# Kernel optimization log

Measured on AMD Instinct MI355X. Metric: run time of the kernel, lower is better.

Reference implementation:

```python
import jax, jax.numpy as jnp
import numpy as np

EPS = 1e-06


def setup_inputs() -> dict:
    key = jax.random.key(0)
    k1, k2, k3 = jax.random.split(key, 3)
    N, L, H, D = 2, 2048, 8, 64
    return {
        "queries": jax.random.normal(k1, (N, L, H, D), dtype=jnp.float32),
        "keys": jax.random.normal(k2, (N, L, H, D), dtype=jnp.float32),
        "values": jax.random.normal(k3, (N, L, H, D), dtype=jnp.float32),
    }


def reference(queries, keys, values):
    # [N, L, H, D] -> [N, H, L, D]
    q = jnp.transpose(queries, (0, 2, 1, 3))
    k = jnp.transpose(keys, (0, 2, 1, 3))
    v = jnp.transpose(values, (0, 2, 1, 3))
    # kernel_method = sigmoid (applied to q and k only)
    q = jax.nn.sigmoid(q)
    k = jax.nn.sigmoid(k)
    L = q.shape[2]
    normal = (jnp.arange(L, dtype=q.dtype) + 1.0)[None, None, :]  # [1,1,L]

    sink_incoming = 1.0 / jnp.einsum('nhld,nhld->nhl', q + EPS, jnp.cumsum(k, axis=2) + EPS)
    source_outgoing = 1.0 / jnp.einsum('nhld,nhld->nhl', k + EPS, jnp.cumsum(q, axis=2) + EPS)
    sink_incoming = sink_incoming * normal
    source_outgoing = source_outgoing * normal

    conserved_sink = jnp.einsum(
        'nhld,nhld->nhl', q + EPS,
        jnp.cumsum(k * source_outgoing[..., None], axis=2) + EPS) / normal
    conserved_source = jnp.einsum(
        'nhld,nhld->nhl', k + EPS,
        jnp.cumsum(q * sink_incoming[..., None], axis=2) + EPS) / normal
    conserved_source = jnp.clip(conserved_source, -1.0, 1.0)

    sink_allocation = jax.nn.sigmoid(conserved_sink)
    conserved_source = jnp.exp(conserved_source)
    source_competition = conserved_source / jnp.cumsum(conserved_source, axis=-1) * normal

    # causal dot product: outer-product cumsum as in the original
    q_scaled = q * (sink_incoming / normal)[..., None]
    v_scaled = v * source_competition[..., None]
    kv = jnp.cumsum(jnp.einsum('nhld,nhlm->nhldm', k, v_scaled), axis=2)  # [N,H,L,D,M]
    qkv = jnp.einsum('nhld,nhldm->nhlm', q_scaled, kv)
    x = qkv * sink_allocation[..., None]
    # back to [N, L, H, M]
    return jnp.transpose(x, (0, 2, 1, 3))
```

## Files before the change

### kernel.cpp

```cpp
#include <hip/hip_runtime.h>
#include <math.h>

constexpr int Nn = 2, Hh = 8, Ll = 2048, Dd = 64;
constexpr int S  = Nn * Hh;
constexpr int C  = 64;
constexpr int NC = Ll / C;
constexpr int SC = S * NC;

constexpr int SB  = 72;
constexpr int SRP = 65;
constexpr int SS8 = 9;

#define EPSF 1e-6f
#define FLAG_MAGIC 0x5F3A9D21u

typedef __attribute__((ext_vector_type(8))) short short8;
typedef __attribute__((ext_vector_type(4))) float f32x4;
#define MFMA16(a, b, c) __builtin_amdgcn_mfma_f32_16x16x32_bf16(a, b, c, 0, 0, 0)

__device__ __forceinline__ float rcpf(float x) { return __builtin_amdgcn_rcpf(x); }
__device__ __forceinline__ float sigf(float x) { return rcpf(1.0f + __expf(-x)); }

__device__ __forceinline__ float waveRed(float v) {
#pragma unroll
    for (int off = 32; off > 0; off >>= 1) v += __shfl_xor(v, off, 64);
    return v;
}

__device__ __forceinline__ int gidx(int n, int l, int h, int d) {
    return ((n * Ll + l) * Hh + h) * Dd + d;
}

__device__ __forceinline__ float fc(const float4& v, int u) { return ((const float*)&v)[u]; }

__device__ __forceinline__ unsigned short f2bf(float x) {
    unsigned int u = __float_as_uint(x);
    unsigned int r = (u + 0x7fffu + ((u >> 16) & 1u)) >> 16;
    return (unsigned short)r;
}
__device__ __forceinline__ unsigned int pack2(float lo, float hi) {
    return (unsigned int)f2bf(lo) | ((unsigned int)f2bf(hi) << 16);
}
__device__ __forceinline__ float bf2f(unsigned short u) {
    return __uint_as_float(((unsigned int)u) << 16);
}
__device__ __forceinline__ float lo16(unsigned int x) { return __uint_as_float(x << 16); }
__device__ __forceinline__ float hi16(unsigned int x) { return __uint_as_float(x & 0xffff0000u); }
__device__ __forceinline__ void unpack8(const uint4& v, float* o) {
    o[0] = lo16(v.x); o[1] = hi16(v.x); o[2] = lo16(v.y); o[3] = hi16(v.y);
    o[4] = lo16(v.z); o[5] = hi16(v.z); o[6] = lo16(v.w); o[7] = hi16(v.w);
}

__device__ __forceinline__ void pubf(float* p, float v) {
    __hip_atomic_store((unsigned int*)p, __float_as_uint(v),
                       __ATOMIC_RELAXED, __HIP_MEMORY_SCOPE_AGENT);
}
__device__ __forceinline__ float rdf(const float* p) {
    return __uint_as_float(__hip_atomic_load((const unsigned int*)p,
                       __ATOMIC_RELAXED, __HIP_MEMORY_SCOPE_AGENT));
}
__device__ __forceinline__ void pubu(unsigned int* p, unsigned int v) {
    __hip_atomic_store(p, v, __ATOMIC_RELAXED, __HIP_MEMORY_SCOPE_AGENT);
}
__device__ __forceinline__ unsigned long long rd64(const void* p) {
    return __hip_atomic_load((const unsigned long long*)p,
                             __ATOMIC_RELAXED, __HIP_MEMORY_SCOPE_AGENT);
}
__device__ __forceinline__ void publish_flag(unsigned int* f, int t) {
    asm volatile("s_waitcnt vmcnt(0)" ::: "memory");
    __syncthreads();
    if (t == 0)
        __hip_atomic_store(f, FLAG_MAGIC, __ATOMIC_RELAXED, __HIP_MEMORY_SCOPE_AGENT);
}
__device__ __forceinline__ void wait_n(const unsigned int* f, int n, int t) {
    if (t < 64) {
        const bool need = (t < n);
        for (;;) {
            unsigned int v = need
                ? __hip_atomic_load(&f[t], __ATOMIC_RELAXED, __HIP_MEMORY_SCOPE_AGENT)
                : FLAG_MAGIC;
            if (__all(v == FLAG_MAGIC)) break;
            __builtin_amdgcn_s_sleep(8);
        }
    }
    __syncthreads();
    asm volatile("" ::: "memory");
}

__global__ __launch_bounds__(256, 2) void k_all(
        const float* __restrict__ Q, const float* __restrict__ K,
        const float* __restrict__ V,
        float* __restrict__ SK, float* __restrict__ SQ,
        float* __restrict__ SKso, float* __restrict__ SQsi,
        float* __restrict__ KVT, unsigned short* __restrict__ KVpb,
        float* __restrict__ Out,
        unsigned int* __restrict__ f0, unsigned int* __restrict__ f1,
        unsigned long long* __restrict__ f2, unsigned int* __restrict__ f3,
        unsigned int* __restrict__ f4) {
    __shared__ __align__(16) unsigned short sqB[C * SB];
    __shared__ __align__(16) unsigned short skB[C * SB];
    __shared__ __align__(16) unsigned short vsT[C * SB];
    __shared__ __align__(16) unsigned short stB[C * SB];
    __shared__ __align__(16) float Pun[4608];
    __shared__ float scrA[C * SS8], scrB[C * SS8];
    __shared__ float colK[C], colQ[C], pk[Dd], pq[Dd];
    __shared__ float lsi[C], lso[C], rw1[C], rw2[C], le[C], ecum[C], lsc[C], s2l[C];
    __shared__ float pcsv;

    const int b = blockIdx.x, s = b / NC, c = b % NC;
    const int n = s / Hh, h = s % Hh, t = threadIdx.x;
    const int w = t >> 6, lane = t & 63, mf = lane & 15, qq = lane >> 4;
    const int I0 = 16 * w;
    float* P = Pun;

    {
        int d0 = (4 * t) & 63, ig = t >> 4;
        float psk[4] = {0, 0, 0, 0}, psq[4] = {0, 0, 0, 0};
#pragma unroll
        for (int j = 0; j < 4; j++) {
            int i = ig + 16 * j;
            int id = gidx(n, c * C + i, h, d0);
            float4 q4 = *(const float4*)&Q[id];
            float4 k4 = *(const float4*)&K[id];
            float a0 = sigf(q4.x), a1 = sigf(q4.y), a2 = sigf(q4.z), a3 = sigf(q4.w);
            float b0 = sigf(k4.x), b1 = sigf(k4.y), b2 = sigf(k4.z), b3 = sigf(k4.w);
            *(uint2*)&sqB[i * SB + d0] = make_uint2(pack2(a0, a1), pack2(a2, a3));
            *(uint2*)&skB[i * SB + d0] = make_uint2(pack2(b0, b1), pack2(b2, b3));
            psq[0] += a0; psq[1] += a1; psq[2] += a2; psq[3] += a3;
            psk[0] += b0; psk[1] += b1; psk[2] += b2; psk[3] += b3;
        }
#pragma unroll
        for (int r = 0; r < 4; r++) {
            P[ig * 64 + d0 + r] = psk[r];
            P[1024 + ig * 64 + d0 + r] = psq[r];
        }
        int i0 = (t & 15) * 4, dt = (t >> 4) * 4;
        float4 vr[4];
#pragma unroll
        for (int r = 0; r < 4; r++)
            vr[r] = *(const float4*)&V[gidx(n, c * C + i0 + r, h, dt)];
#pragma unroll
        for (int u = 0; u < 4; u++)
            *(uint2*)&vsT[(dt + u) * SB + i0] = make_uint2(
                pack2(fc(vr[0], u), fc(vr[1], u)), pack2(fc(vr[2], u), fc(vr[3], u)));
    }
    __syncthreads();
    if (t < 64) {
        float v = 0.f;
#pragma unroll
        for (int g = 0; g < 16; g++) v += P[g * 64 + t];
        pubf(&SK[b * 64 + t], v);
    } else if (t < 128) {
        int d = t - 64; float v = 0.f;
#pragma unroll
        for (int g = 0; g < 16; g++) v += P[1024 + g * 64 + d];
        pubf(&SQ[b * 64 + d], v);
    }
    publish_flag(&f0[b], t);

    wait_n(&f0[s * NC], c, t);

    {
        int d = t & 63, g = t >> 6;
        float pa = 0.f, pb = 0.f;
#pragma unroll
        for (int u = 0; u < 8; u++) {
            int cp = g + 4 * u;
            float va = rdf(&SK[(s * NC + cp) * 64 + d]);
            float vb = rdf(&SQ[(s * NC + cp) * 64 + d]);
            pa += (cp < c) ? va : 0.f;
            pb += (cp < c) ? vb : 0.f;
        }
        P[2048 + g * 64 + d] = pa;
        P[2304 + g * 64 + d] = pb;
    }
#pragma unroll
    for (int j = 0; j < 2; j++) {
        int flat = 8 * t + 2048 * j, i = flat >> 6, d0 = flat & 63;
        uint4 xq = *(const uint4*)&sqB[i * SB + d0];
        uint4 xk = *(const uint4*)&skB[i * SB + d0];
        float qa[8], ka[8];
        unpack8(xq, qa); unpack8(xk, ka);
        float sq = 0.f, sk = 0.f;
#pragma unroll
        for (int u = 0; u < 8; u++) { sq += qa[u]; sk += ka[u]; }
        scrB[i * SS8 + (d0 >> 3)] = sq;
        scrA[i * SS8 + (d0 >> 3)] = sk;
    }
    __syncthreads();
    if (t < 64) {
        float v = 0.f;
#pragma unroll
        for (int u = 0; u < 8; u++) v += scrA[t * SS8 + u];
        colK[t] = v;
    } else if (t < 128) {
        int i = t - 64; float v = 0.f;
#pragma unroll
        for (int u = 0; u < 8; u++) v += scrB[i * SS8 + u];
        colQ[i] = v;
    } else if (t < 192) {
        int d = t - 128;
        pk[d] = P[2048 + d] + P[2112 + d] + P[2176 + d] + P[2240 + d];
    } else {
        int d = t - 192;
        pq[d] = P[2304 + d] + P[2368 + d] + P[2432 + d] + P[2496 + d];
    }
    __syncthreads();

    {
        f32x4 acc[4] = {{0,0,0,0},{0,0,0,0},{0,0,0,0},{0,0,0,0}};
#pragma unroll
        for (int kk = 0; kk < 64; kk += 32) {
            short8 a = *(const short8*)&sqB[(I0 + mf) * SB + kk + qq * 8];
#pragma unroll
            for (int J = 0; J < 4; J++) {
                short8 bb = *(const short8*)&skB[(16 * J + mf) * SB + kk + qq * 8];
                acc[J] = MFMA16(a, bb, acc[J]);
            }
        }
#pragma unroll
        for (int J = 0; J < 4; J++)
#pragma unroll
            for (int r = 0; r < 4; r++)
                P[(I0 + 4 * qq + r) * SRP + 16 * J + mf] = acc[J][r];
    }
    __syncthreads();

    {
        int i = t >> 2, g = t & 3, l = c * C + i;
        float prow[16], pcol[16];
        float r1 = 0.f, r2 = 0.f;
#pragma unroll
        for (int u = 0; u < 16; u++) {
            int jj = g + 4 * u;
            prow[u] = P[i * SRP + jj] + EPSF * colK[jj];
            pcol[u] = P[jj * SRP + i] + EPSF * colQ[jj];
            bool ok = (jj <= i);
            r1 += ok ? prow[u] : 0.f;
            r2 += ok ? pcol[u] : 0.f;
        }
        float b1 = 0.f, b2 = 0.f;
#pragma unroll
        for (int u = 0; u < 16; u++) {
            int d = g * 16 + u;
            b1 += (bf2f(sqB[i * SB + d]) + EPSF) * (pk[d] + EPSF);
            b2 += (bf2f(skB[i * SB + d]) + EPSF) * (pq[d] + EPSF);
        }
        r1 += __shfl_xor(r1, 1, 64); r1 += __shfl_xor(r1, 2, 64);
        r2 += __shfl_xor(r2, 1, 64); r2 += __shfl_xor(r2, 2, 64);
        b1 += __shfl_xor(b1, 1, 64); b1 += __shfl_xor(b1, 2, 64);
        b2 += __shfl_xor(b2, 1, 64); b2 += __shfl_xor(b2, 2, 64);
        if (g == 0) {
            float nf = (float)(l + 1);
            lsi[i] = nf * rcpf(b1 + r1);
            lso[i] = nf * rcpf(b2 + r2);
        }
        __syncthreads();

        float a1 = 0.f, a2 = 0.f;
#pragma unroll
        for (int u = 0; u < 16; u++) {
            int jj = g + 4 * u;
            float t1 = lso[jj] * prow[u];
            float t2 = lsi[jj] * pcol[u];
            bool ok = (jj <= i);
            a1 += ok ? t1 : 0.f;
            a2 += ok ? t2 : 0.f;
        }
        a1 += __shfl_xor(a1, 1, 64); a1 += __shfl_xor(a1, 2, 64);
        a2 += __shfl_xor(a2, 1, 64); a2 += __shfl_xor(a2, 2, 64);
        if (g == 0) { rw1[i] = a1; rw2[i] = a2; }
    }
    {
        int d = t >> 2, g = t & 3;
        float v1 = 0.f, v2 = 0.f;
#pragma unroll
        for (int u = 0; u < 16; u++) {
            int i = g * 16 + u;
            v1 += bf2f(skB[i * SB + d]) * lso[i];
            v2 += bf2f(sqB[i * SB + d]) * lsi[i];
        }
        v1 += __shfl_xor(v1, 1, 64); v1 += __shfl_xor(v1, 2, 64);
        v2 += __shfl_xor(v2, 1, 64); v2 += __shfl_xor(v2, 2, 64);
        if (g == 0) {
            pubf(&SKso[b * 64 + d], v1);
            pubf(&SQsi[b * 64 + d], v2);
        }
    }
    publish_flag(&f1[b], t);

    wait_n(&f1[s * NC], c, t);

    {
        int d = t & 63, g = t >> 6;
        float pa = 0.f, pb = 0.f;
#pragma unroll
        for (int u = 0; u < 8; u++) {
            int cp = g + 4 * u;
            float va = rdf(&SKso[(s * NC + cp) * 64 + d]);
            float vb = rdf(&SQsi[(s * NC + cp) * 64 + d]);
            pa += (cp < c) ? va : 0.f;
            pb += (cp < c) ? vb : 0.f;
        }
        scrA[g * 64 + d] = pa;
        scrA[256 + g * 64 + d] = pb;
    }
    __syncthreads();
    if (t < 64) pk[t] = scrA[t] + scrA[64 + t] + scrA[128 + t] + scrA[192 + t];
    else if (t < 128) {
        int d = t - 64;
        pq[d] = scrA[256 + d] + scrA[320 + d] + scrA[384 + d] + scrA[448 + d];
    }
    __syncthreads();
    {
        int i = t >> 2, g = t & 3, l = c * C + i;
        float b1 = 0.f, b2 = 0.f;
#pragma unroll
        for (int j = 0; j < 2; j++) {
            uint4 xq = *(const uint4*)&sqB[i * SB + g * 16 + 8 * j];
            uint4 xk = *(const uint4*)&skB[i * SB + g * 16 + 8 * j];
            float qa[8], ka[8];
            unpack8(xq, qa); unpack8(xk, ka);
            int d = g * 16 + 8 * j;
#pragma unroll
            for (int u = 0; u < 8; u++) {
                b1 += (qa[u] + EPSF) * (pk[d + u] + EPSF);
                b2 += (ka[u] + EPSF) * (pq[d + u] + EPSF);
            }
        }
        b1 += __shfl_xor(b1, 1, 64); b1 += __shfl_xor(b1, 2, 64);
        b2 += __shfl_xor(b2, 1, 64); b2 += __shfl_xor(b2, 2, 64);
        if (g == 0) {
            float nf = (float)(l + 1);
            float cs  = (b1 + rw1[i]) * rcpf(nf);
            float csr = (b2 + rw2[i]) * rcpf(nf);
            csr = fminf(fmaxf(csr, -1.f), 1.f);
            float e = __expf(csr);
            float sal = sigf(cs);
            s2l[i] = lsi[i] * rcpf(nf) * sal;
            le[i] = e;
        }
    }
    __syncthreads();
    if (t < 64) {
        float run = le[t];
#pragma unroll
        for (int off = 1; off < 64; off <<= 1) {
            float o = __shfl_up(run, off, 64);
            if (t >= off) run += o;
        }
        ecum[t] = run;
    }
    __syncthreads();
    if (t == 0) {
        unsigned long long pv = ((unsigned long long)FLAG_MAGIC << 32)
                              | (unsigned long long)__float_as_uint(ecum[63]);
        __hip_atomic_store(&f2[b], pv, __ATOMIC_RELAXED, __HIP_MEMORY_SCOPE_AGENT);
    }

    if (t < 64) {
        bool need = (t < c);
        float tv = 0.f;
        for (;;) {
            unsigned long long x = need
                ? __hip_atomic_load(&f2[s * NC + t], __ATOMIC_RELAXED, __HIP_MEMORY_SCOPE_AGENT)
                : ((unsigned long long)FLAG_MAGIC << 32);
            if (__all((unsigned int)(x >> 32) == FLAG_MAGIC)) {
                tv = need ? __uint_as_float((unsigned int)x) : 0.f;
                break;
            }
            __builtin_amdgcn_s_sleep(8);
        }
        float v = waveRed(tv);
        if (t == 0) pcsv = v;
    }
    __syncthreads();

    if (t < 64) {
        int l = c * C + t;
        lsc[t] = le[t] * rcpf(pcsv + ecum[t]) * (float)(l + 1);
    }
    __syncthreads();

    {
        int i = t >> 2, g = t & 3;
        unsigned int wds[8];
#pragma unroll
        for (int p = 0; p < 8; p++) {
            int j0 = g * 16 + 2 * p;
            float v0 = (j0     <= i) ? P[i * SRP + j0]     * lsc[j0]     : 0.f;
            float v1 = (j0 + 1 <= i) ? P[i * SRP + j0 + 1] * lsc[j0 + 1] : 0.f;
            wds[p] = pack2(v0, v1);
        }
        *(uint4*)&stB[i * SB + g * 16]     = make_uint4(wds[0], wds[1], wds[2], wds[3]);
        *(uint4*)&stB[i * SB + g * 16 + 8] = make_uint4(wds[4], wds[5], wds[6], wds[7]);
    }
    __syncthreads();

    unsigned short* skT = (unsigned short*)Pun;
    unsigned short* vsV = (unsigned short*)(Pun + 2304);
#pragma unroll
    for (int j = 0; j < 2; j++) {
        int flat = 8 * t + 2048 * j, dR = flat >> 6, i0 = flat & 63;
        uint4 vv = *(const uint4*)&vsT[dR * SB + i0];
        float x[8];
        unpack8(vv, x);
#pragma unroll
        for (int u = 0; u < 8; u++) x[u] *= lsc[i0 + u];
        uint4 o;
        o.x = pack2(x[0], x[1]); o.y = pack2(x[2], x[3]);
        o.z = pack2(x[4], x[5]); o.w = pack2(x[6], x[7]);
        *(uint4*)&vsV[dR * SB + i0] = o;
    }
    {
        int i0 = (t & 15) * 4, dt = (t >> 4) * 4;
        uint2 kr[4];
#pragma unroll
        for (int r = 0; r < 4; r++) kr[r] = *(const uint2*)&skB[(i0 + r) * SB + dt];
#pragma unroll
        for (int u = 0; u < 4; u++) {
            unsigned int e0 = (u < 2 ? kr[0].x : kr[0].y), e1 = (u < 2 ? kr[1].x : kr[1].y);
            unsigned int e2 = (u < 2 ? kr[2].x : kr[2].y), e3 = (u < 2 ? kr[3].x : kr[3].y);
            int sh = (u & 1) * 16;
            unsigned int lo = ((e0 >> sh) & 0xffffu) | (((e1 >> sh) & 0xffffu) << 16);
            unsigned int hi = ((e2 >> sh) & 0xffffu) | (((e3 >> sh) & 0xffffu) << 16);
            *(uint2*)&skT[(dt + u) * SB + i0] = make_uint2(lo, hi);
        }
    }
    __syncthreads();

    {
        f32x4 acc[4] = {{0,0,0,0},{0,0,0,0},{0,0,0,0},{0,0,0,0}};
#pragma unroll
        for (int kk = 0; kk < 64; kk += 32) {
            short8 a = *(const short8*)&vsV[(I0 + mf) * SB + kk + qq * 8];
#pragma unroll
            for (int J = 0; J < 4; J++) {
                short8 bb = *(const short8*)&skT[(16 * J + mf) * SB + kk + qq * 8];
                acc[J] = MFMA16(a, bb, acc[J]);
            }
        }
#pragma unroll
        for (int J = 0; J < 4; J++)
#pragma unroll
            for (int r = 0; r < 4; r++)
                pubf(&KVT[(size_t)b * 4096 + (I0 + 4 * qq + r) * 64 + 16 * J + mf],
                     acc[J][r]);
    }
    publish_flag(&f3[b], t);

    if (c < 8) {
        wait_n(&f3[s * NC], NC, t);
        int e0 = c * 512 + 2 * t;
        float2 x[NC];
#pragma unroll
        for (int cp = 0; cp < NC; cp++) {
            unsigned long long v = rd64(&KVT[(size_t)(s * NC + cp) * 4096 + e0]);
            x[cp].x = __uint_as_float((unsigned int)v);
            x[cp].y = __uint_as_float((unsigned int)(v >> 32));
        }
        float r0 = 0.f, r1 = 0.f;
#pragma unroll
        for (int cp = 0; cp < NC; cp++) {
            pubu((unsigned int*)&KVpb[(size_t)(s * NC + cp) * 4096 + e0], pack2(r0, r1));
            r0 += x[cp].x; r1 += x[cp].y;
        }
        publish_flag(&f4[s * 8 + c], t);
    }

    wait_n(&f4[8 * s], 8, t);
    unsigned long long kvp[4];
    size_t base = (size_t)b * 4096;
#pragma unroll
    for (int j = 0; j < 2; j++) {
        kvp[2 * j]     = rd64(&KVpb[base + 8 * t + 2048 * j]);
        kvp[2 * j + 1] = rd64(&KVpb[base + 8 * t + 2048 * j + 4]);
    }
#pragma unroll
    for (int j = 0; j < 2; j++) {
        int flat = 8 * t + 2048 * j, i = flat >> 6, d0 = flat & 63;
        *(uint2*)&skB[i * SB + d0] =
            make_uint2((unsigned int)kvp[2 * j], (unsigned int)(kvp[2 * j] >> 32));
        *(uint2*)&skB[i * SB + d0 + 4] =
            make_uint2((unsigned int)kvp[2 * j + 1], (unsigned int)(kvp[2 * j + 1] >> 32));
    }
    __syncthreads();

    {
        f32x4 acc[4] = {{0,0,0,0},{0,0,0,0},{0,0,0,0},{0,0,0,0}};
#pragma unroll
        for (int kk = 0; kk < 64; kk += 32) {
            short8 a1 = *(const short8*)&sqB[(I0 + mf) * SB + kk + qq * 8];
            short8 a2 = *(const short8*)&stB[(I0 + mf) * SB + kk + qq * 8];
#pragma unroll
            for (int J = 0; J < 4; J++) {
                short8 b1 = *(const short8*)&skB[(16 * J + mf) * SB + kk + qq * 8];
                acc[J] = MFMA16(a1, b1, acc[J]);
                short8 b2 = *(const short8*)&vsT[(16 * J + mf) * SB + kk + qq * 8];
                acc[J] = MFMA16(a2, b2, acc[J]);
            }
        }
#pragma unroll
        for (int J = 0; J < 4; J++)
#pragma unroll
            for (int r = 0; r < 4; r++) {
                int io = I0 + 4 * qq + r;
                Out[gidx(n, c * C + io, h, 16 * J + mf)] = acc[J][r] * s2l[io];
            }
    }
}

extern "C" void kernel_launch(void* const* d_in, const int* in_sizes, int n_in,
                              void* d_out, int out_size, void* d_ws, size_t ws_size,
                              hipStream_t stream) {
    const float* Q = (const float*)d_in[0];
    const float* K = (const float*)d_in[1];
    const float* V = (const float*)d_in[2];
    float* Out = (float*)d_out;

    float* ws   = (float*)d_ws;
    float* SK   = ws;
    float* SQ   = SK   + SC * 64;
    float* SKso = SQ   + SC * 64;
    float* SQsi = SKso + SC * 64;
    float* KVT  = SQsi + SC * 64;
    unsigned short* KVpb = (unsigned short*)(KVT + (size_t)SC * 4096);
    unsigned long long* f2 = (unsigned long long*)(KVpb + (size_t)SC * 4096);
    unsigned int* f0 = (unsigned int*)(f2 + SC);
    unsigned int* f1 = f0 + SC;
    unsigned int* f3 = f1 + SC;
    unsigned int* f4 = f3 + SC;

    k_all<<<SC, 256, 0, stream>>>(Q, K, V, SK, SQ, SKso, SQsi, KVT, KVpb, Out,
                                  f0, f1, f2, f3, f4);
}
```

Before: 99.54 us.

## Overlap cross-block flag waits with independent local work

```diff
diff --git a/kernel.cpp b/kernel.cpp
--- a/kernel.cpp
+++ b/kernel.cpp
@@ -134,15 +134,6 @@
             P[ig * 64 + d0 + r] = psk[r];
             P[1024 + ig * 64 + d0 + r] = psq[r];
         }
-        int i0 = (t & 15) * 4, dt = (t >> 4) * 4;
-        float4 vr[4];
-#pragma unroll
-        for (int r = 0; r < 4; r++)
-            vr[r] = *(const float4*)&V[gidx(n, c * C + i0 + r, h, dt)];
-#pragma unroll
-        for (int u = 0; u < 4; u++)
-            *(uint2*)&vsT[(dt + u) * SB + i0] = make_uint2(
-                pack2(fc(vr[0], u), fc(vr[1], u)), pack2(fc(vr[2], u), fc(vr[3], u)));
     }
     __syncthreads();
     if (t < 64) {
@@ -158,22 +149,18 @@
     }
     publish_flag(&f0[b], t);
 
-    wait_n(&f0[s * NC], c, t);
-
-    {
-        int d = t & 63, g = t >> 6;
-        float pa = 0.f, pb = 0.f;
-#pragma unroll
-        for (int u = 0; u < 8; u++) {
-            int cp = g + 4 * u;
-            float va = rdf(&SK[(s * NC + cp) * 64 + d]);
-            float vb = rdf(&SQ[(s * NC + cp) * 64 + d]);
-            pa += (cp < c) ? va : 0.f;
-            pb += (cp < c) ? vb : 0.f;
-        }
-        P[2048 + g * 64 + d] = pa;
-        P[2304 + g * 64 + d] = pb;
-    }
+    {
+        int i0 = (t & 15) * 4, dt = (t >> 4) * 4;
+        float4 vr[4];
+#pragma unroll
+        for (int r = 0; r < 4; r++)
+            vr[r] = *(const float4*)&V[gidx(n, c * C + i0 + r, h, dt)];
+#pragma unroll
+        for (int u = 0; u < 4; u++)
+            *(uint2*)&vsT[(dt + u) * SB + i0] = make_uint2(
+                pack2(fc(vr[0], u), fc(vr[1], u)), pack2(fc(vr[2], u), fc(vr[3], u)));
+    }
+
 #pragma unroll
     for (int j = 0; j < 2; j++) {
         int flat = 8 * t + 2048 * j, i = flat >> 6, d0 = flat & 63;
@@ -198,12 +185,6 @@
 #pragma unroll
         for (int u = 0; u < 8; u++) v += scrB[i * SS8 + u];
         colQ[i] = v;
-    } else if (t < 192) {
-        int d = t - 128;
-        pk[d] = P[2048 + d] + P[2112 + d] + P[2176 + d] + P[2240 + d];
-    } else {
-        int d = t - 192;
-        pq[d] = P[2304 + d] + P[2368 + d] + P[2432 + d] + P[2496 + d];
     }
     __syncthreads();
 
@@ -226,51 +207,61 @@
     }
     __syncthreads();
 
-    {
-        int i = t >> 2, g = t & 3, l = c * C + i;
-        float prow[16], pcol[16];
-        float r1 = 0.f, r2 = 0.f;
+    const int bi = t >> 2, bg = t & 3, bl = c * C + bi;
+    float prow[16], pcol[16];
+    float r1 = 0.f, r2 = 0.f;
+#pragma unroll
+    for (int u = 0; u < 16; u++) {
+        int jj = bg + 4 * u;
+        prow[u] = P[bi * SRP + jj] + EPSF * colK[jj];
+        pcol[u] = P[jj * SRP + bi] + EPSF * colQ[jj];
+        bool ok = (jj <= bi);
+        r1 += ok ? prow[u] : 0.f;
+        r2 += ok ? pcol[u] : 0.f;
+    }
+    r1 += __shfl_xor(r1, 1, 64); r1 += __shfl_xor(r1, 2, 64);
+    r2 += __shfl_xor(r2, 1, 64); r2 += __shfl_xor(r2, 2, 64);
+
+    wait_n(&f0[s * NC], c, t);
+
+    {
+        int d = t & 63, g = t >> 6;
+        float pa = 0.f, pb = 0.f;
+#pragma unroll
+        for (int u = 0; u < 8; u++) {
+            int cp = g + 4 * u;
+            float va = rdf(&SK[(s * NC + cp) * 64 + d]);
+            float vb = rdf(&SQ[(s * NC + cp) * 64 + d]);
+            pa += (cp < c) ? va : 0.f;
+            pb += (cp < c) ? vb : 0.f;
+        }
+        scrA[g * 64 + d] = pa;
+        scrA[256 + g * 64 + d] = pb;
+    }
+    __syncthreads();
+    if (t < 64) pk[t] = scrA[t] + scrA[64 + t] + scrA[128 + t] + scrA[192 + t];
+    else if (t < 128) {
+        int d = t - 64;
+        pq[d] = scrA[256 + d] + scrA[320 + d] + scrA[384 + d] + scrA[448 + d];
+    }
+    __syncthreads();
+    {
+        float b1 = 0.f, b2 = 0.f;
 #pragma unroll
         for (int u = 0; u < 16; u++) {
-            int jj = g + 4 * u;
-            prow[u] = P[i * SRP + jj] + EPSF * colK[jj];
-            pcol[u] = P[jj * SRP + i] + EPSF * colQ[jj];
-            bool ok = (jj <= i);
-            r1 += ok ? prow[u] : 0.f;
-            r2 += ok ? pcol[u] : 0.f;
-        }
-        float b1 = 0.f, b2 = 0.f;
-#pragma unroll
-        for (int u = 0; u < 16; u++) {
-            int d = g * 16 + u;
-            b1 += (bf2f(sqB[i * SB + d]) + EPSF) * (pk[d] + EPSF);
-            b2 += (bf2f(skB[i * SB + d]) + EPSF) * (pq[d] + EPSF);
-        }
-        r1 += __shfl_xor(r1, 1, 64); r1 += __shfl_xor(r1, 2, 64);
-        r2 += __shfl_xor(r2, 1, 64); r2 += __shfl_xor(r2, 2, 64);
+            int d = bg * 16 + u;
+            b1 += (bf2f(sqB[bi * SB + d]) + EPSF) * (pk[d] + EPSF);
+            b2 += (bf2f(skB[bi * SB + d]) + EPSF) * (pq[d] + EPSF);
+        }
         b1 += __shfl_xor(b1, 1, 64); b1 += __shfl_xor(b1, 2, 64);
         b2 += __shfl_xor(b2, 1, 64); b2 += __shfl_xor(b2, 2, 64);
-        if (g == 0) {
-            float nf = (float)(l + 1);
-            lsi[i] = nf * rcpf(b1 + r1);
-            lso[i] = nf * rcpf(b2 + r2);
-        }
-        __syncthreads();
-
-        float a1 = 0.f, a2 = 0.f;
-#pragma unroll
-        for (int u = 0; u < 16; u++) {
-            int jj = g + 4 * u;
-            float t1 = lso[jj] * prow[u];
-            float t2 = lsi[jj] * pcol[u];
-            bool ok = (jj <= i);
-            a1 += ok ? t1 : 0.f;
-            a2 += ok ? t2 : 0.f;
-        }
-        a1 += __shfl_xor(a1, 1, 64); a1 += __shfl_xor(a1, 2, 64);
-        a2 += __shfl_xor(a2, 1, 64); a2 += __shfl_xor(a2, 2, 64);
-        if (g == 0) { rw1[i] = a1; rw2[i] = a2; }
-    }
+        if (bg == 0) {
+            float nf = (float)(bl + 1);
+            lsi[bi] = nf * rcpf(b1 + r1);
+            lso[bi] = nf * rcpf(b2 + r2);
+        }
+    }
+    __syncthreads();
     {
         int d = t >> 2, g = t & 3;
         float v1 = 0.f, v2 = 0.f;
@@ -288,6 +279,22 @@
         }
     }
     publish_flag(&f1[b], t);
+
+    {
+        float a1 = 0.f, a2 = 0.f;
+#pragma unroll
+        for (int u = 0; u < 16; u++) {
+            int jj = bg + 4 * u;
+            float t1 = lso[jj] * prow[u];
+            float t2 = lsi[jj] * pcol[u];
+            bool ok = (jj <= bi);
+            a1 += ok ? t1 : 0.f;
+            a2 += ok ? t2 : 0.f;
+        }
+        a1 += __shfl_xor(a1, 1, 64); a1 += __shfl_xor(a1, 2, 64);
+        a2 += __shfl_xor(a2, 1, 64); a2 += __shfl_xor(a2, 2, 64);
+        if (bg == 0) { rw1[bi] = a1; rw2[bi] = a2; }
+    }
 
     wait_n(&f1[s * NC], c, t);
 
@@ -313,15 +320,14 @@
     }
     __syncthreads();
     {
-        int i = t >> 2, g = t & 3, l = c * C + i;
         float b1 = 0.f, b2 = 0.f;
 #pragma unroll
         for (int j = 0; j < 2; j++) {
-            uint4 xq = *(const uint4*)&sqB[i * SB + g * 16 + 8 * j];
-            uint4 xk = *(const uint4*)&skB[i * SB + g * 16 + 8 * j];
+            uint4 xq = *(const uint4*)&sqB[bi * SB + bg * 16 + 8 * j];
+            uint4 xk = *(const uint4*)&skB[bi * SB + bg * 16 + 8 * j];
             float qa[8], ka[8];
             unpack8(xq, qa); unpack8(xk, ka);
-            int d = g * 16 + 8 * j;
+            int d = bg * 16 + 8 * j;
 #pragma unroll
             for (int u = 0; u < 8; u++) {
                 b1 += (qa[u] + EPSF) * (pk[d + u] + EPSF);
@@ -330,15 +336,15 @@
         }
         b1 += __shfl_xor(b1, 1, 64); b1 += __shfl_xor(b1, 2, 64);
         b2 += __shfl_xor(b2, 1, 64); b2 += __shfl_xor(b2, 2, 64);
-        if (g == 0) {
-            float nf = (float)(l + 1);
-            float cs  = (b1 + rw1[i]) * rcpf(nf);
-            float csr = (b2 + rw2[i]) * rcpf(nf);
+        if (bg == 0) {
+            float nf = (float)(bl + 1);
+            float cs  = (b1 + rw1[bi]) * rcpf(nf);
+            float csr = (b2 + rw2[bi]) * rcpf(nf);
             csr = fminf(fmaxf(csr, -1.f), 1.f);
             float e = __expf(csr);
             float sal = sigf(cs);
-            s2l[i] = lsi[i] * rcpf(nf) * sal;
-            le[i] = e;
+            s2l[bi] = lsi[bi] * rcpf(nf) * sal;
+            le[bi] = e;
         }
     }
     __syncthreads();
@@ -375,6 +381,7 @@
         if (t == 0) pcsv = v;
     }
     __syncthreads();
+    asm volatile("" ::: "memory");
 
     if (t < 64) {
         int l = c * C + t;
@@ -459,55 +466,62 @@
             x[cp].x = __uint_as_float((unsigned int)v);
             x[cp].y = __uint_as_float((unsigned int)(v >> 32));
         }
-        float r0 = 0.f, r1 = 0.f;
+        float r0 = 0.f, r1p = 0.f;
 #pragma unroll
         for (int cp = 0; cp < NC; cp++) {
-            pubu((unsigned int*)&KVpb[(size_t)(s * NC + cp) * 4096 + e0], pack2(r0, r1));
-            r0 += x[cp].x; r1 += x[cp].y;
+            pubu((unsigned int*)&KVpb[(size_t)(s * NC + cp) * 4096 + e0], pack2(r0, r1p));
+            r0 += x[cp].x; r1p += x[cp].y;
         }
         publish_flag(&f4[s * 8 + c], t);
     }
 
+    f32x4 acc[4] = {{0,0,0,0},{0,0,0,0},{0,0,0,0},{0,0,0,0}};
+#pragma unroll
+    for (int kk = 0; kk < 64; kk += 32) {
+        short8 a2 = *(const short8*)&stB[(I0 + mf) * SB + kk + qq * 8];
+#pragma unroll
+        for (int J = 0; J < 4; J++) {
+            short8 b2 = *(const short8*)&vsT[(16 * J + mf) * SB + kk + qq * 8];
+            acc[J] = MFMA16(a2, b2, acc[J]);
+        }
+    }
+
     wait_n(&f4[8 * s], 8, t);
-    unsigned long long kvp[4];
-    size_t base = (size_t)b * 4096;
-#pragma unroll
-    for (int j = 0; j < 2; j++) {
-        kvp[2 * j]     = rd64(&KVpb[base + 8 * t + 2048 * j]);
-        kvp[2 * j + 1] = rd64(&KVpb[base + 8 * t + 2048 * j + 4]);
-    }
-#pragma unroll
-    for (int j = 0; j < 2; j++) {
-        int flat = 8 * t + 2048 * j, i = flat >> 6, d0 = flat & 63;
-        *(uint2*)&skB[i * SB + d0] =
-            make_uint2((unsigned int)kvp[2 * j], (unsigned int)(kvp[2 * j] >> 32));
-        *(uint2*)&skB[i * SB + d0 + 4] =
-            make_uint2((unsigned int)kvp[2 * j + 1], (unsigned int)(kvp[2 * j + 1] >> 32));
-    }
-    __syncthreads();
-
-    {
-        f32x4 acc[4] = {{0,0,0,0},{0,0,0,0},{0,0,0,0},{0,0,0,0}};
-#pragma unroll
-        for (int kk = 0; kk < 64; kk += 32) {
-            short8 a1 = *(const short8*)&sqB[(I0 + mf) * SB + kk + qq * 8];
-            short8 a2 = *(const short8*)&stB[(I0 + mf) * SB + kk + qq * 8];
-#pragma unroll
-            for (int J = 0; J < 4; J++) {
-                short8 b1 = *(const short8*)&skB[(16 * J + mf) * SB + kk + qq * 8];
-                acc[J] = MFMA16(a1, b1, acc[J]);
-                short8 b2 = *(const short8*)&vsT[(16 * J + mf) * SB + kk + qq * 8];
-                acc[J] = MFMA16(a2, b2, acc[J]);
-            }
-        }
-#pragma unroll
-        for (int J = 0; J < 4; J++)
-#pragma unroll
-            for (int r = 0; r < 4; r++) {
-                int io = I0 + 4 * qq + r;
-                Out[gidx(n, c * C + io, h, 16 * J + mf)] = acc[J][r] * s2l[io];
-            }
-    }
+    {
+        unsigned long long kvp[4];
+        size_t base = (size_t)b * 4096;
+#pragma unroll
+        for (int j = 0; j < 2; j++) {
+            kvp[2 * j]     = rd64(&KVpb[base + 8 * t + 2048 * j]);
+            kvp[2 * j + 1] = rd64(&KVpb[base + 8 * t + 2048 * j + 4]);
+        }
+#pragma unroll
+        for (int j = 0; j < 2; j++) {
+            int flat = 8 * t + 2048 * j, i = flat >> 6, d0 = flat & 63;
+            *(uint2*)&skB[i * SB + d0] =
+                make_uint2((unsigned int)kvp[2 * j], (unsigned int)(kvp[2 * j] >> 32));
+            *(uint2*)&skB[i * SB + d0 + 4] =
+                make_uint2((unsigned int)kvp[2 * j + 1], (unsigned int)(kvp[2 * j + 1] >> 32));
+        }
+    }
+    __syncthreads();
+
+#pragma unroll
+    for (int kk = 0; kk < 64; kk += 32) {
+        short8 a1 = *(const short8*)&sqB[(I0 + mf) * SB + kk + qq * 8];
+#pragma unroll
+        for (int J = 0; J < 4; J++) {
+            short8 b1 = *(const short8*)&skB[(16 * J + mf) * SB + kk + qq * 8];
+            acc[J] = MFMA16(a1, b1, acc[J]);
+        }
+    }
+#pragma unroll
+    for (int J = 0; J < 4; J++)
+#pragma unroll
+        for (int r = 0; r < 4; r++) {
+            int io = I0 + 4 * qq + r;
+            Out[gidx(n, c * C + io, h, 16 * J + mf)] = acc[J][r] * s2l[io];
+        }
 }
 
 extern "C" void kernel_launch(void* const* d_in, const int* in_sizes, int n_in,
```

Measured after the change: 96.39 us. 1.03x faster.
